# Optimization experiments

Measured on AMD Instinct MI355X. Metric: run time of the kernel, lower is better.

Reference implementation:

```python
import jax, jax.numpy as jnp
import numpy as np


def setup_inputs() -> dict:
    key = jax.random.key(0)
    ks = jax.random.split(key, 9)
    B, H = 8192, 1024
    scale = 1.0 / np.sqrt(4 * H)
    return {
        "h": jax.random.normal(ks[0], (B, H), jnp.float32),
        "x": jax.random.normal(ks[1], (B, 2 * H), jnp.float32),
        "glo": jax.random.normal(ks[2], (B, H), jnp.float32),
        "Wi_w": jax.random.normal(ks[3], (H, 4 * H), jnp.float32) * scale,
        "Wi_b": jnp.zeros((H,), jnp.float32),
        "Wf_w": jax.random.normal(ks[4], (H, 4 * H), jnp.float32) * scale,
        "Wf_b": jnp.zeros((H,), jnp.float32),
        "Wc_w": jax.random.normal(ks[5], (H, 4 * H), jnp.float32) * scale,
        "Wc_b": jnp.zeros((H,), jnp.float32),
    }


def reference(h, x, glo, Wi_w, Wi_b, Wf_w, Wf_b, Wc_w, Wc_b):
    # Dropout is identity in eval mode (deterministic reference).
    cat_all = jnp.concatenate([h, x, glo], axis=-1)  # [B, 4H]
    # Fused gate GEMM: stack the three weight matrices, one matmul.
    W = jnp.concatenate([Wi_w, Wf_w, Wc_w], axis=0)      # [3H, 4H]
    b = jnp.concatenate([Wi_b, Wf_b, Wc_b], axis=0)      # [3H]
    gates = cat_all @ W.T + b                             # [B, 3H]
    H = h.shape[-1]
    i = jax.nn.sigmoid(gates[:, :H])
    f = jax.nn.sigmoid(gates[:, H:2 * H])
    c = jnp.tanh(gates[:, 2 * H:])
    # 2-way softmax over (i, f): alpha0 = exp(i)/(exp(i)+exp(f)) = sigmoid(i-f)
    alpha0 = jax.nn.sigmoid(i - f)
    output = alpha0 * c + (1.0 - alpha0) * h
    return output
```

## Files before the change

kernel.cpp:

```cpp
#include <hip/hip_runtime.h>

typedef unsigned short USHORT;
typedef short bf16x8 __attribute__((ext_vector_type(8)));
typedef float f32x4 __attribute__((ext_vector_type(4)));

__device__ __forceinline__ USHORT f2bf(float f) {
    unsigned u = __float_as_uint(f);
    u += 0x7fffu + ((u >> 16) & 1u);
    return (USHORT)(u >> 16);
}
__device__ __forceinline__ float bf2f(USHORT s) {
    return __uint_as_float(((unsigned)s) << 16);
}
__device__ __forceinline__ float sigm(float v) { return 1.f / (1.f + __expf(-v)); }
__device__ __forceinline__ float mytanh(float v) { return 1.f - 2.f / (__expf(2.f * v) + 1.f); }

using gcu32p = const unsigned int __attribute__((address_space(1))) *;
using lu32p  = unsigned int __attribute__((address_space(3))) *;

__device__ __forceinline__ void load_lds16(const void* g, void* l) {
    __builtin_amdgcn_global_load_lds((gcu32p)g, (lu32p)l, 16, 0, 0);
}

__global__ __launch_bounds__(256) void conv_A(const float* __restrict__ h,
                                              const float* __restrict__ x,
                                              const float* __restrict__ glo,
                                              USHORT* __restrict__ A) {
    int idx = (blockIdx.x * 256 + threadIdx.x) * 8;
    int m = idx >> 12, k = idx & 4095;
    const float* s;
    if (k < 1024)      s = h   + (size_t)m * 1024 + k;
    else if (k < 3072) s = x   + (size_t)m * 2048 + (k - 1024);
    else               s = glo + (size_t)m * 1024 + (k - 3072);
    float4 f0 = ((const float4*)s)[0];
    float4 f1 = ((const float4*)s)[1];
    union { USHORT us[8]; uint4 v; } u;
    u.us[0] = f2bf(f0.x); u.us[1] = f2bf(f0.y); u.us[2] = f2bf(f0.z); u.us[3] = f2bf(f0.w);
    u.us[4] = f2bf(f1.x); u.us[5] = f2bf(f1.y); u.us[6] = f2bf(f1.z); u.us[7] = f2bf(f1.w);
    *(uint4*)(A + idx) = u.v;
}

__global__ __launch_bounds__(256) void conv_W(const float* __restrict__ Wi,
                                              const float* __restrict__ Wf,
                                              const float* __restrict__ Wc,
                                              USHORT* __restrict__ W) {
    int idx = (blockIdx.x * 256 + threadIdx.x) * 8;
    int n = idx >> 12, k = idx & 4095;
    const float* base = (n < 1024) ? Wi : (n < 2048 ? Wf : Wc);
    const float* s = base + (size_t)(n & 1023) * 4096 + k;
    float4 f0 = ((const float4*)s)[0];
    float4 f1 = ((const float4*)s)[1];
    union { USHORT us[8]; uint4 v; } u;
    u.us[0] = f2bf(f0.x); u.us[1] = f2bf(f0.y); u.us[2] = f2bf(f0.z); u.us[3] = f2bf(f0.w);
    u.us[4] = f2bf(f1.x); u.us[5] = f2bf(f1.y); u.us[6] = f2bf(f1.z); u.us[7] = f2bf(f1.w);
    *(uint4*)(W + idx) = u.v;
}

__global__ __launch_bounds__(256) void gemm_bt(const USHORT* __restrict__ A,
                                               const USHORT* __restrict__ B,
                                               const float* __restrict__ bi,
                                               const float* __restrict__ bfp,
                                               const float* __restrict__ bc,
                                               USHORT* __restrict__ gates) {
    __shared__ USHORT At[128 * 32];
    __shared__ USHORT Bt[128 * 32];

    const int tid  = threadIdx.x;
    const int lane = tid & 63, wv = tid >> 6;
    const int bx = blockIdx.x;
    const int n0 = bx * 128;
    const int m0 = blockIdx.y * 128;
    const int wM = wv >> 1, wN = wv & 1;
    const int lm = lane & 15, qk = (lane >> 4) * 8;

    const int eA0 = wv * 512 + lane * 8;
    const int eA1 = (4 + wv) * 512 + lane * 8;
    USHORT* lA0 = At + wv * 512;
    USHORT* lA1 = At + (4 + wv) * 512;
    USHORT* lB0 = Bt + wv * 512;
    USHORT* lB1 = Bt + (4 + wv) * 512;

    const USHORT* a0 = A + (size_t)(m0 + (eA0 >> 5)) * 4096 + (eA0 & 31);
    const USHORT* a1 = A + (size_t)(m0 + (eA1 >> 5)) * 4096 + (eA1 & 31);
    const USHORT* b0 = B + (size_t)(n0 + (eA0 >> 5)) * 4096 + (eA0 & 31);
    const USHORT* b1 = B + (size_t)(n0 + (eA1 >> 5)) * 4096 + (eA1 & 31);

    f32x4 acc[4][4];
    #pragma unroll
    for (int a = 0; a < 4; ++a)
        #pragma unroll
        for (int b = 0; b < 4; ++b) {
            f32x4 z = {0.f, 0.f, 0.f, 0.f};
            acc[a][b] = z;
        }

    for (int kt = 0; kt < 128; ++kt) {
        __syncthreads();
        load_lds16(a0, lA0);
        load_lds16(a1, lA1);
        load_lds16(b0, lB0);
        load_lds16(b1, lB1);
        a0 += 32; a1 += 32; b0 += 32; b1 += 32;
        __syncthreads();

        bf16x8 av[4], bv[4];
        #pragma unroll
        for (int mt = 0; mt < 4; ++mt)
            av[mt] = *(const bf16x8*)(At + (wM * 64 + mt * 16 + lm) * 32 + qk);
        #pragma unroll
        for (int nt = 0; nt < 4; ++nt)
            bv[nt] = *(const bf16x8*)(Bt + (wN * 64 + nt * 16 + lm) * 32 + qk);
        #pragma unroll
        for (int mt = 0; mt < 4; ++mt)
            #pragma unroll
            for (int nt = 0; nt < 4; ++nt)
                acc[mt][nt] = __builtin_amdgcn_mfma_f32_16x16x32_bf16(
                    av[mt], bv[nt], acc[mt][nt], 0, 0, 0);
    }

    const float* bias = (bx < 8) ? bi : (bx < 16 ? bfp : bc);
    const int boff = (bx & 7) * 128;
    #pragma unroll
    for (int nt = 0; nt < 4; ++nt) {
        int lcol = wN * 64 + nt * 16 + lm;
        float bb = bias[boff + lcol];
        #pragma unroll
        for (int mt = 0; mt < 4; ++mt) {
            #pragma unroll
            for (int r = 0; r < 4; ++r) {
                int lrow = wM * 64 + mt * 16 + (lane >> 4) * 4 + r;
                gates[(size_t)(m0 + lrow) * 3072 + n0 + lcol] = f2bf(acc[mt][nt][r] + bb);
            }
        }
    }
}

__global__ __launch_bounds__(256) void epi(const USHORT* __restrict__ gates,
                                           const float* __restrict__ h,
                                           float* __restrict__ out) {
    int e = (blockIdx.x * 256 + threadIdx.x) * 8;
    int m = e >> 10, n = e & 1023;
    const USHORT* gp = gates + (size_t)m * 3072 + n;
    union { USHORT us[8]; uint4 v; } gi, gf, gc;
    gi.v = *(const uint4*)(gp);
    gf.v = *(const uint4*)(gp + 1024);
    gc.v = *(const uint4*)(gp + 2048);
    const float* hp = h + (size_t)m * 1024 + n;
    float4 h0 = ((const float4*)hp)[0];
    float4 h1 = ((const float4*)hp)[1];
    float hv[8] = {h0.x, h0.y, h0.z, h0.w, h1.x, h1.y, h1.z, h1.w};
    float o[8];
    #pragma unroll
    for (int j = 0; j < 8; ++j) {
        float iv = sigm(bf2f(gi.us[j]));
        float fv = sigm(bf2f(gf.us[j]));
        float cv = mytanh(bf2f(gc.us[j]));
        float al = sigm(iv - fv);
        o[j] = al * cv + (1.f - al) * hv[j];
    }
    float4* op = (float4*)(out + (size_t)m * 1024 + n);
    op[0] = make_float4(o[0], o[1], o[2], o[3]);
    op[1] = make_float4(o[4], o[5], o[6], o[7]);
}

template <bool PRECONV>
__global__ __launch_bounds__(256) void gemm3(const USHORT* __restrict__ Abf,
                                             const USHORT* __restrict__ Wbf,
                                             const float* __restrict__ h,
                                             const float* __restrict__ x,
                                             const float* __restrict__ glo,
                                             const float* __restrict__ Wi,
                                             const float* __restrict__ Wf,
                                             const float* __restrict__ Wc,
                                             const float* __restrict__ bi,
                                             const float* __restrict__ bfp,
                                             const float* __restrict__ bc,
                                             float* __restrict__ out) {
    __shared__ USHORT At[128 * 32];
    __shared__ USHORT Bt[128 * 32];
    __shared__ USHORT stash[128 * 136];

    const int tid  = threadIdx.x;
    const int lane = tid & 63, wv = tid >> 6;
    const int n0 = blockIdx.x * 128;
    const int m0 = blockIdx.y * 128;
    const int wM = wv >> 1, wN = wv & 1;
    const int lm = lane & 15, qk = (lane >> 4) * 8;

    const int eA0 = wv * 512 + lane * 8;
    const int eA1 = (4 + wv) * 512 + lane * 8;
    USHORT* lA0 = At + wv * 512;
    USHORT* lA1 = At + (4 + wv) * 512;
    USHORT* lB0 = Bt + wv * 512;
    USHORT* lB1 = Bt + (4 + wv) * 512;

    const USHORT* gA0base = nullptr;
    const USHORT* gA1base = nullptr;
    if constexpr (PRECONV) {
        gA0base = Abf + (size_t)(m0 + (eA0 >> 5)) * 4096 + (eA0 & 31);
        gA1base = Abf + (size_t)(m0 + (eA1 >> 5)) * 4096 + (eA1 & 31);
    }
    const int rowS = tid >> 1;
    const int colS = (tid & 1) * 16;

    for (int p = 0; p < 3; ++p) {
        f32x4 acc[4][4];
        #pragma unroll
        for (int a = 0; a < 4; ++a)
            #pragma unroll
            for (int b = 0; b < 4; ++b) {
                f32x4 z = {0.f, 0.f, 0.f, 0.f};
                acc[a][b] = z;
            }

        const USHORT* a0 = gA0base;
        const USHORT* a1 = gA1base;
        const USHORT* b0 = nullptr;
        const USHORT* b1 = nullptr;
        const float* Wg = nullptr;
        if constexpr (PRECONV) {
            b0 = Wbf + ((size_t)p * 1024 + n0 + (eA0 >> 5)) * 4096 + (eA0 & 31);
            b1 = Wbf + ((size_t)p * 1024 + n0 + (eA1 >> 5)) * 4096 + (eA1 & 31);
        } else {
            Wg = (p == 0) ? Wi : (p == 1 ? Wf : Wc);
        }

        for (int kt = 0; kt < 128; ++kt) {
            __syncthreads();
            if constexpr (PRECONV) {
                load_lds16(a0, lA0);
                load_lds16(a1, lA1);
                load_lds16(b0, lB0);
                load_lds16(b1, lB1);
                a0 += 32; a1 += 32; b0 += 32; b1 += 32;
            } else {
                int k = kt * 32 + colS;
                const float* s;
                if (k < 1024)      s = h   + (size_t)(m0 + rowS) * 1024 + k;
                else if (k < 3072) s = x   + (size_t)(m0 + rowS) * 2048 + (k - 1024);
                else               s = glo + (size_t)(m0 + rowS) * 1024 + (k - 3072);
                float4 f0 = ((const float4*)s)[0], f1 = ((const float4*)s)[1];
                float4 f2 = ((const float4*)s)[2], f3 = ((const float4*)s)[3];
                union { USHORT us[8]; uint4 v; } u0, u1;
                u0.us[0]=f2bf(f0.x); u0.us[1]=f2bf(f0.y); u0.us[2]=f2bf(f0.z); u0.us[3]=f2bf(f0.w);
                u0.us[4]=f2bf(f1.x); u0.us[5]=f2bf(f1.y); u0.us[6]=f2bf(f1.z); u0.us[7]=f2bf(f1.w);
                u1.us[0]=f2bf(f2.x); u1.us[1]=f2bf(f2.y); u1.us[2]=f2bf(f2.z); u1.us[3]=f2bf(f2.w);
                u1.us[4]=f2bf(f3.x); u1.us[5]=f2bf(f3.y); u1.us[6]=f2bf(f3.z); u1.us[7]=f2bf(f3.w);
                *(uint4*)(At + rowS * 32 + colS)     = u0.v;
                *(uint4*)(At + rowS * 32 + colS + 8) = u1.v;
                const float* sw = Wg + (size_t)(n0 + rowS) * 4096 + k;
                float4 w0 = ((const float4*)sw)[0], w1 = ((const float4*)sw)[1];
                float4 w2 = ((const float4*)sw)[2], w3 = ((const float4*)sw)[3];
                union { USHORT us[8]; uint4 v; } v0, v1;
                v0.us[0]=f2bf(w0.x); v0.us[1]=f2bf(w0.y); v0.us[2]=f2bf(w0.z); v0.us[3]=f2bf(w0.w);
                v0.us[4]=f2bf(w1.x); v0.us[5]=f2bf(w1.y); v0.us[6]=f2bf(w1.z); v0.us[7]=f2bf(w1.w);
                v1.us[0]=f2bf(w2.x); v1.us[1]=f2bf(w2.y); v1.us[2]=f2bf(w2.z); v1.us[3]=f2bf(w2.w);
                v1.us[4]=f2bf(w3.x); v1.us[5]=f2bf(w3.y); v1.us[6]=f2bf(w3.z); v1.us[7]=f2bf(w3.w);
                *(uint4*)(Bt + rowS * 32 + colS)     = v0.v;
                *(uint4*)(Bt + rowS * 32 + colS + 8) = v1.v;
            }
            __syncthreads();

            bf16x8 av[4], bv[4];
            #pragma unroll
            for (int mt = 0; mt < 4; ++mt)
                av[mt] = *(const bf16x8*)(At + (wM * 64 + mt * 16 + lm) * 32 + qk);
            #pragma unroll
            for (int nt = 0; nt < 4; ++nt)
                bv[nt] = *(const bf16x8*)(Bt + (wN * 64 + nt * 16 + lm) * 32 + qk);
            #pragma unroll
            for (int mt = 0; mt < 4; ++mt)
                #pragma unroll
                for (int nt = 0; nt < 4; ++nt)
                    acc[mt][nt] = __builtin_amdgcn_mfma_f32_16x16x32_bf16(
                        av[mt], bv[nt], acc[mt][nt], 0, 0, 0);
        }

        const float* bias = (p == 0) ? bi : (p == 1 ? bfp : bc);
        #pragma unroll
        for (int nt = 0; nt < 4; ++nt) {
            int lcol = wN * 64 + nt * 16 + lm;
            float bb = bias[n0 + lcol];
            #pragma unroll
            for (int mt = 0; mt < 4; ++mt) {
                #pragma unroll
                for (int r = 0; r < 4; ++r) {
                    int lrow = wM * 64 + mt * 16 + (lane >> 4) * 4 + r;
                    float g = acc[mt][nt][r] + bb;
                    int li = lrow * 136 + lcol;
                    if (p == 0) {
                        stash[li] = f2bf(sigm(g));
                    } else if (p == 1) {
                        float iv = bf2f(stash[li]);
                        stash[li] = f2bf(sigm(iv - sigm(g)));
                    } else {
                        float al = bf2f(stash[li]);
                        float cv = mytanh(g);
                        size_t gi = (size_t)(m0 + lrow) * 1024 + (n0 + lcol);
                        out[gi] = al * cv + (1.f - al) * h[gi];
                    }
                }
            }
        }
    }
}

extern "C" void kernel_launch(void* const* d_in, const int* in_sizes, int n_in,
                              void* d_out, int out_size, void* d_ws, size_t ws_size,
                              hipStream_t stream) {
    const float* h   = (const float*)d_in[0];
    const float* x   = (const float*)d_in[1];
    const float* glo = (const float*)d_in[2];
    const float* Wi  = (const float*)d_in[3];
    const float* bi  = (const float*)d_in[4];
    const float* Wf  = (const float*)d_in[5];
    const float* bfp = (const float*)d_in[6];
    const float* Wc  = (const float*)d_in[7];
    const float* bc  = (const float*)d_in[8];
    float* out = (float*)d_out;

    const size_t szA = (size_t)8192 * 4096 * 2;
    const size_t szW = (size_t)3072 * 4096 * 2;
    const size_t szG = (size_t)8192 * 3072 * 2;

    if (ws_size >= szA + szW + szG) {
        USHORT* Abf = (USHORT*)d_ws;
        USHORT* Wbf = (USHORT*)((char*)d_ws + szA);
        USHORT* Gbf = (USHORT*)((char*)d_ws + szA + szW);
        conv_A<<<16384, 256, 0, stream>>>(h, x, glo, Abf);
        conv_W<<<6144, 256, 0, stream>>>(Wi, Wf, Wc, Wbf);
        gemm_bt<<<dim3(24, 64), 256, 0, stream>>>(Abf, Wbf, bi, bfp, bc, Gbf);
        epi<<<4096, 256, 0, stream>>>(Gbf, h, out);
    } else if (ws_size >= szA + szW) {
        USHORT* Abf = (USHORT*)d_ws;
        USHORT* Wbf = (USHORT*)((char*)d_ws + szA);
        conv_A<<<16384, 256, 0, stream>>>(h, x, glo, Abf);
        conv_W<<<6144, 256, 0, stream>>>(Wi, Wf, Wc, Wbf);
        gemm3<true><<<dim3(8, 64), 256, 0, stream>>>(
            Abf, Wbf, h, x, glo, nullptr, nullptr, nullptr, bi, bfp, bc, out);
    } else {
        gemm3<false><<<dim3(8, 64), 256, 0, stream>>>(
            nullptr, nullptr, h, x, glo, Wi, Wf, Wc, bi, bfp, bc, out);
    }
}
```

Before: 451.3 us.

## Swizzle LDS tile layout in GEMM and merge conversion kernels into one launch

The GEMM's global-to-LDS load mapping now places each 16-byte k-group at a position XOR-swizzled by row, and the fragment reads apply the matching swizzle. This is meant to cut LDS bank conflicts when the MFMA operands are read. Separately, the two fp32-to-bf16 conversion kernels are merged into one launch that branches on block index, saving one kernel launch and its tail. If the swizzle on the write side and the read side do not match exactly, results will be wrong.

```diff
diff --git a/kernel.cpp b/kernel.cpp
--- a/kernel.cpp
+++ b/kernel.cpp
@@ -22,38 +22,40 @@
     __builtin_amdgcn_global_load_lds((gcu32p)g, (lu32p)l, 16, 0, 0);
 }
 
-__global__ __launch_bounds__(256) void conv_A(const float* __restrict__ h,
-                                              const float* __restrict__ x,
-                                              const float* __restrict__ glo,
-                                              USHORT* __restrict__ A) {
-    int idx = (blockIdx.x * 256 + threadIdx.x) * 8;
-    int m = idx >> 12, k = idx & 4095;
-    const float* s;
-    if (k < 1024)      s = h   + (size_t)m * 1024 + k;
-    else if (k < 3072) s = x   + (size_t)m * 2048 + (k - 1024);
-    else               s = glo + (size_t)m * 1024 + (k - 3072);
-    float4 f0 = ((const float4*)s)[0];
-    float4 f1 = ((const float4*)s)[1];
-    union { USHORT us[8]; uint4 v; } u;
-    u.us[0] = f2bf(f0.x); u.us[1] = f2bf(f0.y); u.us[2] = f2bf(f0.z); u.us[3] = f2bf(f0.w);
-    u.us[4] = f2bf(f1.x); u.us[5] = f2bf(f1.y); u.us[6] = f2bf(f1.z); u.us[7] = f2bf(f1.w);
-    *(uint4*)(A + idx) = u.v;
-}
-
-__global__ __launch_bounds__(256) void conv_W(const float* __restrict__ Wi,
-                                              const float* __restrict__ Wf,
-                                              const float* __restrict__ Wc,
-                                              USHORT* __restrict__ W) {
-    int idx = (blockIdx.x * 256 + threadIdx.x) * 8;
-    int n = idx >> 12, k = idx & 4095;
-    const float* base = (n < 1024) ? Wi : (n < 2048 ? Wf : Wc);
-    const float* s = base + (size_t)(n & 1023) * 4096 + k;
-    float4 f0 = ((const float4*)s)[0];
-    float4 f1 = ((const float4*)s)[1];
-    union { USHORT us[8]; uint4 v; } u;
-    u.us[0] = f2bf(f0.x); u.us[1] = f2bf(f0.y); u.us[2] = f2bf(f0.z); u.us[3] = f2bf(f0.w);
-    u.us[4] = f2bf(f1.x); u.us[5] = f2bf(f1.y); u.us[6] = f2bf(f1.z); u.us[7] = f2bf(f1.w);
-    *(uint4*)(W + idx) = u.v;
+__global__ __launch_bounds__(256) void conv_all(const float* __restrict__ h,
+                                                const float* __restrict__ x,
+                                                const float* __restrict__ glo,
+                                                const float* __restrict__ Wi,
+                                                const float* __restrict__ Wf,
+                                                const float* __restrict__ Wc,
+                                                USHORT* __restrict__ A,
+                                                USHORT* __restrict__ W) {
+    int bid = blockIdx.x;
+    if (bid < 16384) {
+        int idx = (bid * 256 + threadIdx.x) * 8;
+        int m = idx >> 12, k = idx & 4095;
+        const float* s;
+        if (k < 1024)      s = h   + (size_t)m * 1024 + k;
+        else if (k < 3072) s = x   + (size_t)m * 2048 + (k - 1024);
+        else               s = glo + (size_t)m * 1024 + (k - 3072);
+        float4 f0 = ((const float4*)s)[0];
+        float4 f1 = ((const float4*)s)[1];
+        union { USHORT us[8]; uint4 v; } u;
+        u.us[0] = f2bf(f0.x); u.us[1] = f2bf(f0.y); u.us[2] = f2bf(f0.z); u.us[3] = f2bf(f0.w);
+        u.us[4] = f2bf(f1.x); u.us[5] = f2bf(f1.y); u.us[6] = f2bf(f1.z); u.us[7] = f2bf(f1.w);
+        *(uint4*)(A + idx) = u.v;
+    } else {
+        int idx = ((bid - 16384) * 256 + threadIdx.x) * 8;
+        int n = idx >> 12, k = idx & 4095;
+        const float* base = (n < 1024) ? Wi : (n < 2048 ? Wf : Wc);
+        const float* s = base + (size_t)(n & 1023) * 4096 + k;
+        float4 f0 = ((const float4*)s)[0];
+        float4 f1 = ((const float4*)s)[1];
+        union { USHORT us[8]; uint4 v; } u;
+        u.us[0] = f2bf(f0.x); u.us[1] = f2bf(f0.y); u.us[2] = f2bf(f0.z); u.us[3] = f2bf(f0.w);
+        u.us[4] = f2bf(f1.x); u.us[5] = f2bf(f1.y); u.us[6] = f2bf(f1.z); u.us[7] = f2bf(f1.w);
+        *(uint4*)(W + idx) = u.v;
+    }
 }
 
 __global__ __launch_bounds__(256) void gemm_bt(const USHORT* __restrict__ A,
@@ -71,19 +73,21 @@
     const int n0 = bx * 128;
     const int m0 = blockIdx.y * 128;
     const int wM = wv >> 1, wN = wv & 1;
-    const int lm = lane & 15, qk = (lane >> 4) * 8;
-
-    const int eA0 = wv * 512 + lane * 8;
-    const int eA1 = (4 + wv) * 512 + lane * 8;
+    const int lm = lane & 15;
+    const int gw = lane >> 4;
+    const int swz8 = (gw ^ ((lm >> 1) & 3)) * 8;
+
+    const int rS = wv * 16 + (lane >> 2);
+    const int gS = (lane & 3) ^ ((rS >> 1) & 3);
     USHORT* lA0 = At + wv * 512;
     USHORT* lA1 = At + (4 + wv) * 512;
     USHORT* lB0 = Bt + wv * 512;
     USHORT* lB1 = Bt + (4 + wv) * 512;
 
-    const USHORT* a0 = A + (size_t)(m0 + (eA0 >> 5)) * 4096 + (eA0 & 31);
-    const USHORT* a1 = A + (size_t)(m0 + (eA1 >> 5)) * 4096 + (eA1 & 31);
-    const USHORT* b0 = B + (size_t)(n0 + (eA0 >> 5)) * 4096 + (eA0 & 31);
-    const USHORT* b1 = B + (size_t)(n0 + (eA1 >> 5)) * 4096 + (eA1 & 31);
+    const USHORT* a0 = A + (size_t)(m0 + rS) * 4096 + gS * 8;
+    const USHORT* a1 = A + (size_t)(m0 + rS + 64) * 4096 + gS * 8;
+    const USHORT* b0 = B + (size_t)(n0 + rS) * 4096 + gS * 8;
+    const USHORT* b1 = B + (size_t)(n0 + rS + 64) * 4096 + gS * 8;
 
     f32x4 acc[4][4];
     #pragma unroll
@@ -106,10 +110,10 @@
         bf16x8 av[4], bv[4];
         #pragma unroll
         for (int mt = 0; mt < 4; ++mt)
-            av[mt] = *(const bf16x8*)(At + (wM * 64 + mt * 16 + lm) * 32 + qk);
+            av[mt] = *(const bf16x8*)(At + (wM * 64 + mt * 16 + lm) * 32 + swz8);
         #pragma unroll
         for (int nt = 0; nt < 4; ++nt)
-            bv[nt] = *(const bf16x8*)(Bt + (wN * 64 + nt * 16 + lm) * 32 + qk);
+            bv[nt] = *(const bf16x8*)(Bt + (wN * 64 + nt * 16 + lm) * 32 + swz8);
         #pragma unroll
         for (int mt = 0; mt < 4; ++mt)
             #pragma unroll
@@ -327,15 +331,13 @@
         USHORT* Abf = (USHORT*)d_ws;
         USHORT* Wbf = (USHORT*)((char*)d_ws + szA);
         USHORT* Gbf = (USHORT*)((char*)d_ws + szA + szW);
-        conv_A<<<16384, 256, 0, stream>>>(h, x, glo, Abf);
-        conv_W<<<6144, 256, 0, stream>>>(Wi, Wf, Wc, Wbf);
+        conv_all<<<16384 + 6144, 256, 0, stream>>>(h, x, glo, Wi, Wf, Wc, Abf, Wbf);
         gemm_bt<<<dim3(24, 64), 256, 0, stream>>>(Abf, Wbf, bi, bfp, bc, Gbf);
         epi<<<4096, 256, 0, stream>>>(Gbf, h, out);
     } else if (ws_size >= szA + szW) {
         USHORT* Abf = (USHORT*)d_ws;
         USHORT* Wbf = (USHORT*)((char*)d_ws + szA);
-        conv_A<<<16384, 256, 0, stream>>>(h, x, glo, Abf);
-        conv_W<<<6144, 256, 0, stream>>>(Wi, Wf, Wc, Wbf);
+        conv_all<<<16384 + 6144, 256, 0, stream>>>(h, x, glo, Wi, Wf, Wc, Abf, Wbf);
         gemm3<true><<<dim3(8, 64), 256, 0, stream>>>(
             Abf, Wbf, h, x, glo, nullptr, nullptr, nullptr, bi, bfp, bc, out);
     } else {
```

Measured after the change: 448.8 us. About the same (-0.6%).
